# Optimization experiments

Hardware: AMD Instinct MI355X
Metric: run time of the kernel (lower is better)

The kernel has to match this reference:

```python
import jax, jax.numpy as jnp
import numpy as np

POS_THR = 0.5
NEG_THR = 0.4
WEIGHTS = (1.0, 1.0, 1.0, 1.0)


def _box_iou(a, b):
    # a: (N,4), b: (M,4) in xyxy -> (N,M) IoU
    area_a = (a[:, 2] - a[:, 0]) * (a[:, 3] - a[:, 1])  # (N,)
    area_b = (b[:, 2] - b[:, 0]) * (b[:, 3] - b[:, 1])  # (M,)
    lt = jnp.maximum(a[:, None, :2], b[None, :, :2])  # (N,M,2)
    rb = jnp.minimum(a[:, None, 2:], b[None, :, 2:])  # (N,M,2)
    wh = jnp.clip(rb - lt, 0.0)
    inter = wh[..., 0] * wh[..., 1]  # (N,M)
    return inter / (area_a[:, None] + area_b[None, :] - inter)


def _encode(anchors, gt):
    # both (N,4) xyxy -> (N,4) deltas (dx,dy,dw,dh)
    eps = jnp.finfo(jnp.float32).eps
    ax = (anchors[:, 0] + anchors[:, 2]) * 0.5
    ay = (anchors[:, 1] + anchors[:, 3]) * 0.5
    aw = jnp.maximum(anchors[:, 2] - anchors[:, 0], eps)
    ah = jnp.maximum(anchors[:, 3] - anchors[:, 1], eps)
    gx = (gt[:, 0] + gt[:, 2]) * 0.5
    gy = (gt[:, 1] + gt[:, 3]) * 0.5
    gw = gt[:, 2] - gt[:, 0]
    gh = gt[:, 3] - gt[:, 1]
    dx = (gx - ax) / aw
    dy = (gy - ay) / ah
    dw = jnp.log(gw / aw)
    dh = jnp.log(gh / ah)
    w = jnp.asarray(WEIGHTS, dtype=jnp.float32)
    return jnp.stack((dx, dy, dw, dh), axis=-1) * w


def setup_inputs() -> dict:
    key = jax.random.key(0)
    k1, k2, k3, k4, k5 = jax.random.split(key, 5)
    N, M, IMG = 200000, 128, 1024.0
    # valid anchor boxes: random centers + sizes in [8, 512]
    ac = jax.random.uniform(k1, (N, 2), dtype=jnp.float32) * IMG
    asz = 8.0 + jax.random.uniform(k2, (N, 2), dtype=jnp.float32) * 504.0
    anchors = jnp.concatenate([ac - 0.5 * asz, ac + 0.5 * asz], axis=-1)
    gc = jax.random.uniform(k3, (M, 2), dtype=jnp.float32) * IMG
    gsz = 16.0 + jax.random.uniform(k4, (M, 2), dtype=jnp.float32) * 480.0
    gt_boxes = jnp.concatenate([gc - 0.5 * gsz, gc + 0.5 * gsz], axis=-1)
    gt_labels = jax.random.randint(k5, (M,), 1, 81, dtype=jnp.int64 if jax.config.jax_enable_x64 else jnp.int32)
    return {"anchors": anchors, "gt_boxes": gt_boxes, "gt_labels": gt_labels}


def reference(anchors, gt_boxes, gt_labels):
    iou = _box_iou(anchors, gt_boxes)  # (N,M)
    max_iou_per_anchor = iou.max(axis=1)              # (N,)
    matched_gt_idx = iou.argmax(axis=1)               # (N,)
    matched_anchor_per_gt = iou.argmax(axis=0)        # (M,)
    pos_mask = max_iou_per_anchor >= POS_THR
    pos_mask = pos_mask.at[matched_anchor_per_gt].set(True)  # force best anchor per gt positive
    neg_mask = (max_iou_per_anchor < NEG_THR) & (~pos_mask)
    cls_targets = jnp.where(pos_mask, gt_labels[matched_gt_idx].astype(jnp.int32),
                            jnp.where(neg_mask, 0, -1))
    enc = _encode(anchors, gt_boxes[matched_gt_idx])  # (N,4)
    reg_targets = jnp.where(pos_mask[:, None], enc, 0.0)
    return cls_targets, reg_targets, pos_mask
```

## Files before the change

kernel.cpp:

```cpp
#include <hip/hip_runtime.h>
#include <cmath>
#include <cstdint>

typedef unsigned long long ull;

constexpr float POS_THR = 0.5f;
constexpr float NEG_THR = 0.4f;
constexpr float F32_EPS = 1.1920928955078125e-07f;

__device__ __forceinline__ float iou_one(const float4 a, const float area_a,
                                         const float4 g, const float area_g) {
    float lx = fmaxf(a.x, g.x);
    float ly = fmaxf(a.y, g.y);
    float rx = fminf(a.z, g.z);
    float ry = fminf(a.w, g.w);
    float w  = fmaxf(rx - lx, 0.0f);
    float h  = fmaxf(ry - ly, 0.0f);
    float inter = w * h;
    return inter / (area_a + area_g - inter);
}

__device__ __forceinline__ float4 encode_box(const float4 a, const float4 g) {
    float ax = (a.x + a.z) * 0.5f;
    float ay = (a.y + a.w) * 0.5f;
    float aw = fmaxf(a.z - a.x, F32_EPS);
    float ah = fmaxf(a.w - a.y, F32_EPS);
    float gx = (g.x + g.z) * 0.5f;
    float gy = (g.y + g.w) * 0.5f;
    float gw = g.z - g.x;
    float gh = g.w - g.y;
    return make_float4((gx - ax) / aw, (gy - ay) / ah, logf(gw / aw), logf(gh / ah));
}

__device__ __forceinline__ ull shfl_xor_u64(ull key, int off) {
    unsigned lo = (unsigned)key;
    unsigned hi = (unsigned)(key >> 32);
    lo = __shfl_xor(lo, off, 64);
    hi = __shfl_xor(hi, off, 64);
    return ((ull)hi << 32) | lo;
}

__global__ __launch_bounds__(256) void fused_kernel(
    const float4* __restrict__ anchors, const float4* __restrict__ gts,
    const int* __restrict__ labels, int n, int m, int nblocks,
    float* __restrict__ out_cls, float4* __restrict__ out_reg,
    float* __restrict__ out_pos, ull* __restrict__ ws)
{
    __shared__ float4 sA[128];
    __shared__ float  sAa[128];
    __shared__ float4 sG[128];
    __shared__ float  sGa[128];
    __shared__ float  sLab[128];
    __shared__ ull    ck[256];

    const int t = threadIdx.x;
    const int base = blockIdx.x * 128;

    if (t < 128) {
        int i = base + t;
        float4 a = make_float4(0.0f, 0.0f, 0.0f, 0.0f);
        if (i < n) a = anchors[i];
        sA[t]  = a;
        sAa[t] = (a.z - a.x) * (a.w - a.y);
    } else {
        int j = t - 128;
        float4 g = gts[j];
        sG[j]  = g;
        sGa[j] = (g.z - g.x) * (g.w - g.y);
        sLab[j] = (float)labels[j];
    }
    __syncthreads();

    const int al = t & 127;
    const int h  = t >> 7;

    {
        float4 a = sA[al];
        float area_a = sAa[al];
        const int j0 = h * 64;
        ull kA = 0ull, kB = 0ull;
        #pragma unroll 4
        for (int k = 0; k < 32; ++k) {
            int jA = j0 + k;
            int jB = j0 + 32 + k;
            float vA = iou_one(a, area_a, sG[jA], sGa[jA]);
            float vB = iou_one(a, area_a, sG[jB], sGa[jB]);
            ull xA = ((ull)__float_as_uint(vA) << 32) | (ull)(~(unsigned)jA);
            ull xB = ((ull)__float_as_uint(vB) << 32) | (ull)(~(unsigned)jB);
            if (xA > kA) kA = xA;
            if (xB > kB) kB = xB;
        }
        ck[t] = kA > kB ? kA : kB;
    }
    __syncthreads();
    if (t < 128) {
        int i = base + t;
        ull k0 = ck[t], k1 = ck[t + 128];
        ull kk = k0 > k1 ? k0 : k1;
        if (i < n) {
            float best = __uint_as_float((unsigned)(kk >> 32));
            int bestj  = (int)(~(unsigned)(kk & 0xFFFFFFFFull));
            bool pos = best >= POS_THR;
            bool neg = (best < NEG_THR) && !pos;
            out_cls[i] = pos ? sLab[bestj] : (neg ? 0.0f : -1.0f);
            out_pos[i] = pos ? 1.0f : 0.0f;
            float4 enc = make_float4(0.0f, 0.0f, 0.0f, 0.0f);
            if (pos) enc = encode_box(sA[t], sG[bestj]);
            out_reg[i] = enc;
        }
    }
    __syncthreads();

    {
        float4 g = sG[al];
        float area_g = sGa[al];
        const int i0 = h * 64;
        ull kA = 0ull, kB = 0ull;
        #pragma unroll 4
        for (int k = 0; k < 32; ++k) {
            int iA = i0 + k;
            int iB = i0 + 32 + k;
            float vA = iou_one(sA[iA], sAa[iA], g, area_g);
            float vB = iou_one(sA[iB], sAa[iB], g, area_g);
            ull xA = ((ull)__float_as_uint(vA) << 32) | (ull)(~(unsigned)(base + iA));
            ull xB = ((ull)__float_as_uint(vB) << 32) | (ull)(~(unsigned)(base + iB));
            if (xA > kA) kA = xA;
            if (xB > kB) kB = xB;
        }
        ck[t] = kA > kB ? kA : kB;
    }
    __syncthreads();
    if (t < 128) {
        ull k0 = ck[t], k1 = ck[t + 128];
        ws[(size_t)t * nblocks + blockIdx.x] = k0 > k1 ? k0 : k1;
    }
}

__global__ __launch_bounds__(256) void reduce_fixup(
    const float4* __restrict__ anchors, const float4* __restrict__ gts,
    const int* __restrict__ labels, int n, int m, int nblocks,
    float* __restrict__ out_cls, float4* __restrict__ out_reg,
    float* __restrict__ out_pos, const ull* __restrict__ ws)
{
    __shared__ ull wk[4];
    __shared__ ull s_winner;
    const int j = blockIdx.x;
    const int t = threadIdx.x;
    const ull* wj = ws + (size_t)j * nblocks;

    ull key = 0ull;
    for (int b = t; b < nblocks; b += 256) {
        ull k = wj[b];
        if (k > key) key = k;
    }
    #pragma unroll
    for (int off = 32; off > 0; off >>= 1) {
        ull o = shfl_xor_u64(key, off);
        if (o > key) key = o;
    }
    if ((t & 63) == 0) wk[t >> 6] = key;
    __syncthreads();
    if (t == 0) {
        ull k = wk[0];
        #pragma unroll
        for (int w = 1; w < 4; ++w) if (wk[w] > k) k = wk[w];
        s_winner = k;
    }
    __syncthreads();
    const unsigned gi = ~(unsigned)(s_winner & 0xFFFFFFFFull);

    if (t < 64) {
        float4 a = anchors[gi];
        float area_a = (a.z - a.x) * (a.w - a.y);
        ull k2 = 0ull;
        for (int jj = t; jj < m; jj += 64) {
            float4 g = gts[jj];
            float area_g = (g.z - g.x) * (g.w - g.y);
            float v = iou_one(a, area_a, g, area_g);
            ull kk = ((ull)__float_as_uint(v) << 32) | (ull)(~(unsigned)jj);
            if (kk > k2) k2 = kk;
        }
        #pragma unroll
        for (int off = 32; off > 0; off >>= 1) {
            ull o = shfl_xor_u64(k2, off);
            if (o > k2) k2 = o;
        }
        if (t == 0) {
            int bj = (int)(~(unsigned)(k2 & 0xFFFFFFFFull));
            out_pos[gi] = 1.0f;
            out_cls[gi] = (float)labels[bj];
            out_reg[gi] = encode_box(a, gts[bj]);
        }
    }
}

extern "C" void kernel_launch(void* const* d_in, const int* in_sizes, int n_in,
                              void* d_out, int out_size, void* d_ws, size_t ws_size,
                              hipStream_t stream)
{
    const float4* anchors = (const float4*)d_in[0];
    const float4* gts     = (const float4*)d_in[1];
    const int*    labels  = (const int*)d_in[2];
    int n = in_sizes[0] / 4;
    int m = in_sizes[1] / 4;

    float*  out     = (float*)d_out;
    float*  out_cls = out;
    float4* out_reg = (float4*)(out + n);
    float*  out_pos = out + 5 * (size_t)n;
    ull*    ws      = (ull*)d_ws;

    int nblocks = (n + 127) / 128;
    fused_kernel<<<nblocks, 256, 0, stream>>>(anchors, gts, labels, n, m, nblocks,
                                              out_cls, out_reg, out_pos, ws);
    reduce_fixup<<<m, 256, 0, stream>>>(anchors, gts, labels, n, m, nblocks,
                                        out_cls, out_reg, out_pos, ws);
}
```

Before: 110.1 us.

## Compute IoU tile once with 8x8 register blocking for row and column argmax

Replaces the two separate IoU passes (per-anchor max, then per-gt max) with a single 8x8 register-tiled computation per thread, which updates the row and column best values together. Each IoU is now computed once instead of twice, and the gt boxes stay in registers. Partial results are reduced through a padded shared-memory array. In exchange the kernel uses more registers and loses the lowest-index tie-breaking within a thread's 8-element slice for column maxima (strict > keeps the first, which still favors the lower index).

```diff
diff --git a/kernel.cpp b/kernel.cpp
--- a/kernel.cpp
+++ b/kernel.cpp
@@ -49,9 +49,8 @@
     __shared__ float4 sA[128];
     __shared__ float  sAa[128];
     __shared__ float4 sG[128];
-    __shared__ float  sGa[128];
     __shared__ float  sLab[128];
-    __shared__ ull    ck[256];
+    __shared__ ull    sK[128][17];
 
     const int t = threadIdx.x;
     const int base = blockIdx.x * 128;
@@ -64,42 +63,54 @@
         sAa[t] = (a.z - a.x) * (a.w - a.y);
     } else {
         int j = t - 128;
-        float4 g = gts[j];
-        sG[j]  = g;
-        sGa[j] = (g.z - g.x) * (g.w - g.y);
+        sG[j] = gts[j];
         sLab[j] = (float)labels[j];
     }
-    __syncthreads();
-
-    const int al = t & 127;
-    const int h  = t >> 7;
-
-    {
-        float4 a = sA[al];
-        float area_a = sAa[al];
-        const int j0 = h * 64;
-        ull kA = 0ull, kB = 0ull;
-        #pragma unroll 4
-        for (int k = 0; k < 32; ++k) {
-            int jA = j0 + k;
-            int jB = j0 + 32 + k;
-            float vA = iou_one(a, area_a, sG[jA], sGa[jA]);
-            float vB = iou_one(a, area_a, sG[jB], sGa[jB]);
-            ull xA = ((ull)__float_as_uint(vA) << 32) | (ull)(~(unsigned)jA);
-            ull xB = ((ull)__float_as_uint(vB) << 32) | (ull)(~(unsigned)jB);
-            if (xA > kA) kA = xA;
-            if (xB > kB) kB = xB;
-        }
-        ck[t] = kA > kB ? kA : kB;
-    }
-    __syncthreads();
+
+    const int tx = t & 15;
+    const int ty = t >> 4;
+    const int g0 = tx * 8;
+    const int a0 = ty * 8;
+
+    float4 g[8];
+    float  ga[8];
+    #pragma unroll
+    for (int j = 0; j < 8; ++j) {
+        g[j]  = gts[g0 + j];
+        ga[j] = (g[j].z - g[j].x) * (g[j].w - g[j].y);
+    }
+
+    float cbest[8];
+    int   cbi[8];
+    #pragma unroll
+    for (int j = 0; j < 8; ++j) { cbest[j] = -1.0f; cbi[j] = 0; }
+
+    __syncthreads();
+
+    for (int ai = 0; ai < 8; ++ai) {
+        float4 a  = sA[a0 + ai];
+        float  aa = sAa[a0 + ai];
+        float rbest = -1.0f;
+        int   rbj   = 0;
+        #pragma unroll
+        for (int j = 0; j < 8; ++j) {
+            float v = iou_one(a, aa, g[j], ga[j]);
+            if (v > rbest)    { rbest = v;    rbj = j;     }
+            if (v > cbest[j]) { cbest[j] = v; cbi[j] = ai; }
+        }
+        sK[a0 + ai][tx] = ((ull)__float_as_uint(rbest) << 32) |
+                          (ull)(~(unsigned)(g0 + rbj));
+    }
+    __syncthreads();
+
     if (t < 128) {
+        ull k = sK[t][0];
+        #pragma unroll
+        for (int x = 1; x < 16; ++x) { ull o = sK[t][x]; if (o > k) k = o; }
         int i = base + t;
-        ull k0 = ck[t], k1 = ck[t + 128];
-        ull kk = k0 > k1 ? k0 : k1;
         if (i < n) {
-            float best = __uint_as_float((unsigned)(kk >> 32));
-            int bestj  = (int)(~(unsigned)(kk & 0xFFFFFFFFull));
+            float best = __uint_as_float((unsigned)(k >> 32));
+            int bestj  = (int)(~(unsigned)k);
             bool pos = best >= POS_THR;
             bool neg = (best < NEG_THR) && !pos;
             out_cls[i] = pos ? sLab[bestj] : (neg ? 0.0f : -1.0f);
@@ -111,28 +122,18 @@
     }
     __syncthreads();
 
-    {
-        float4 g = sG[al];
-        float area_g = sGa[al];
-        const int i0 = h * 64;
-        ull kA = 0ull, kB = 0ull;
-        #pragma unroll 4
-        for (int k = 0; k < 32; ++k) {
-            int iA = i0 + k;
-            int iB = i0 + 32 + k;
-            float vA = iou_one(sA[iA], sAa[iA], g, area_g);
-            float vB = iou_one(sA[iB], sAa[iB], g, area_g);
-            ull xA = ((ull)__float_as_uint(vA) << 32) | (ull)(~(unsigned)(base + iA));
-            ull xB = ((ull)__float_as_uint(vB) << 32) | (ull)(~(unsigned)(base + iB));
-            if (xA > kA) kA = xA;
-            if (xB > kB) kB = xB;
-        }
-        ck[t] = kA > kB ? kA : kB;
-    }
-    __syncthreads();
+    #pragma unroll
+    for (int j = 0; j < 8; ++j) {
+        sK[g0 + j][ty] = ((ull)__float_as_uint(cbest[j]) << 32) |
+                         (ull)(~(unsigned)(base + a0 + cbi[j]));
+    }
+    __syncthreads();
+
     if (t < 128) {
-        ull k0 = ck[t], k1 = ck[t + 128];
-        ws[(size_t)t * nblocks + blockIdx.x] = k0 > k1 ? k0 : k1;
+        ull k = sK[t][0];
+        #pragma unroll
+        for (int y = 1; y < 16; ++y) { ull o = sK[t][y]; if (o > k) k = o; }
+        ws[(size_t)t * nblocks + blockIdx.x] = k;
     }
 }
 
```

Measured after the change: 90.45 us. -17.8%, faster.
